# Optimization experiments

Hardware: AMD Instinct MI355X
Metric: run time of the kernel (lower is better)

The kernel has to match this reference:

```python
import jax, jax.numpy as jnp
from jax import lax
import numpy as np

B, N_VARS, M_CLAUSES, K_DIM = 1024, 64, 256, 12
MAX_ITER = 12


def setup_inputs() -> dict:
    key = jax.random.key(0)
    k1, k2, k3, k4 = jax.random.split(key, 4)
    z = jax.random.uniform(k1, (B, N_VARS), dtype=jnp.float32)          # input probabilities
    S = jax.random.normal(k2, (M_CLAUSES, N_VARS + 1), dtype=jnp.float32) * 0.2  # learnable clause matrix (col 0 = truth var)
    w = jax.random.uniform(k3, (M_CLAUSES,), dtype=jnp.float32)          # learnable clause weights
    r = jax.random.normal(k4, (B, N_VARS, K_DIM), dtype=jnp.float32)     # random init directions
    return {"z": z, "S": S, "w": w, "r": r, "max_iter": MAX_ITER}


def _mixing(z, S, w, r, max_iter):
    Bsz, n = z.shape
    m, N = S.shape  # N = n + 1 (truth variable is column 0)
    k = r.shape[-1]
    eps = jnp.float32(1e-8)

    # truth direction v_T = e_0
    vT = jnp.zeros((k,), dtype=z.dtype).at[0].set(1.0)

    # random unit directions orthogonal to v_T (zero out component along e_0)
    r_perp = r.at[..., 0].set(0.0)
    r_perp = r_perp / jnp.maximum(jnp.linalg.norm(r_perp, axis=-1, keepdims=True), eps)

    # SATNet init: v_i = -cos(pi z_i) v_T + sin(pi z_i) r_perp_i
    ang = jnp.pi * z
    Vvars = -jnp.cos(ang)[..., None] * vT + jnp.sin(ang)[..., None] * r_perp  # [B,n,k]
    V = jnp.concatenate([jnp.broadcast_to(vT, (Bsz, 1, k)), Vvars], axis=1)   # [B,N,k]

    Sw = S * w[:, None]                       # weighted clause matrix [m,N]
    W = jnp.einsum('mn,bnk->bmk', Sw, V)      # running product Sw @ V, [B,m,k]
    snrm = jnp.sum(Sw * Sw, axis=0)           # ||s_i||^2 per variable, [N]

    def coord_step(carry, i):
        V, W = carry
        s_i = Sw[:, i]                         # [m]
        v_old = V[:, i, :]                     # [B,k]
        g = jnp.einsum('bmk,m->bk', W, s_i) - snrm[i] * v_old
        v_new = -g / jnp.maximum(jnp.linalg.norm(g, axis=-1, keepdims=True), eps)
        W = W + (v_new - v_old)[:, None, :] * s_i[None, :, None]  # rank-1 update
        V = V.at[:, i, :].set(v_new)
        return (V, W), None

    def sweep(carry, _):
        carry, _ = lax.scan(coord_step, carry, jnp.arange(1, N))  # coordinate descent over variables
        return carry, None

    (V, _), _ = lax.scan(sweep, (V, W), None, length=max_iter)

    # output probabilities: z_i = arccos(-v_i . v_T) / pi
    cos = jnp.clip(-V[:, 1:, 0], -1.0 + 1e-6, 1.0 - 1e-6)
    return jnp.arccos(cos) / jnp.pi


def reference(z, S, w, r, max_iter):
    return _mixing(z, S, w, r, max_iter)
```

## Files before the change

### kernel.cpp

```cpp
#include <hip/hip_runtime.h>
#include <math.h>

#define BATCH 1024
#define NV    64
#define MC    256
#define KD    12
#define PI_F  3.14159265358979323846f

#define C0OFF  4096
#define DGAOFF 4160
#define DGBOFF 4224
#define CBUF   4288

typedef float f2  __attribute__((ext_vector_type(2)));
typedef float v4f __attribute__((ext_vector_type(4)));
typedef __attribute__((address_space(3))) float lds_f;

template <int CTRL>
__device__ __forceinline__ float dpp_addf(float x) {
  int y = __builtin_amdgcn_update_dpp(0, __float_as_int(x), CTRL, 0xF, 0xF, true);
  return x + __int_as_float(y);
}
template <int CTRL>
__device__ __forceinline__ float dpp_movf(float x) {
  return __int_as_float(
      __builtin_amdgcn_update_dpp(0, __float_as_int(x), CTRL, 0xF, 0xF, true));
}
__device__ __forceinline__ float readlane63(float x) {
  return __int_as_float(__builtin_amdgcn_readlane(__float_as_int(x), 63));
}
__device__ __forceinline__ float rlane(float x, int i) {
  return __int_as_float(__builtin_amdgcn_readlane(__float_as_int(x), i));
}

template <int IMM>
__device__ __forceinline__ void dsr(v4f& d, unsigned base) {
  asm volatile("ds_read_b128 %0, %1 offset:%2" : "=v"(d) : "v"(base), "i"(IMM));
}

__global__ void compute_C_kernel(const float* __restrict__ S,
                                 const float* __restrict__ w,
                                 float* __restrict__ Cg, int nsplit) {
  const int q = blockIdx.x;
  const int mc = blockIdx.y;
  const int j = threadIdx.x;
  if (j > NV) return;
  const int v = (q + 1) % 64 + 1;
  const int mlen = MC / nsplit;
  const int m0 = mc * mlen;
  float a0 = 0.f, a1 = 0.f, a2 = 0.f, a3 = 0.f;
  for (int m = m0; m < m0 + mlen; m += 4) {
    const float w0 = w[m], w1 = w[m + 1], w2 = w[m + 2], w3 = w[m + 3];
    a0 = fmaf(S[(m + 0) * (NV + 1) + v] * w0 * w0, S[(m + 0) * (NV + 1) + j], a0);
    a1 = fmaf(S[(m + 1) * (NV + 1) + v] * w1 * w1, S[(m + 1) * (NV + 1) + j], a1);
    a2 = fmaf(S[(m + 2) * (NV + 1) + v] * w2 * w2, S[(m + 2) * (NV + 1) + j], a2);
    a3 = fmaf(S[(m + 3) * (NV + 1) + v] * w3 * w3, S[(m + 3) * (NV + 1) + j], a3);
  }
  const float acc = (a0 + a1) + (a2 + a3);
  float* buf = Cg + mc * CBUF;
  const int p1 = (v == 1) ? 64 : (v - 1);
  const int p2 = (v == 1) ? 63 : (v == 2) ? 64 : (v - 2);
  if (j == 0) buf[C0OFF + q] = acc;
  if (j == p1) buf[DGAOFF + (v - 1)] = acc;
  if (j == p2) buf[DGBOFF + (v - 1)] = acc;
  if (j > 0) {
    const int j0 = j - 1;
    const float st = (j == v || j == p1 || j == p2) ? 0.f : acc;
    buf[q * 64 + (j0 & 3) * 16 + (j0 >> 2)] = st;
  }
}

__global__ __launch_bounds__(256, 1) void mixing_kernel(
    const float* __restrict__ z, const float* __restrict__ r,
    const float* __restrict__ Cg, const int* __restrict__ max_iter_p,
    float* __restrict__ out, int nsplit) {
  __shared__ __align__(16) float Ls[CBUF];

  const int t = threadIdx.x;
  const int l = t & 63;
  const int jg = l & 3;
  const int kk = l >> 2;
  const int b = blockIdx.x * 4 + (t >> 6);
  const int max_iter = max_iter_p[0];

  {
    const float4* src = (const float4*)Cg;
    float4* dst = (float4*)Ls;
    for (int idx = t; idx < CBUF / 4; idx += 256) {
      float4 a = src[idx];
      for (int u = 1; u < nsplit; ++u) {
        const float4 p = src[u * (CBUF / 4) + idx];
        a.x += p.x; a.y += p.y; a.z += p.z; a.w += p.w;
      }
      dst[idx] = a;
    }
  }

  const float my_e0 = (kk == 0) ? 1.f : 0.f;

  f2 Vv[8];
  #pragma unroll
  for (int p = 0; p < 8; ++p) {
    #pragma unroll
    for (int h = 0; h < 2; ++h) {
      const int j0 = jg + 8 * p + 4 * h;
      const float zv = z[b * NV + j0];
      float rp = 0.f;
      if (kk >= 1 && kk < KD) rp = r[(b * NV + j0) * KD + kk];
      float ssp = rp * rp;
      ssp += __shfl_xor(ssp, 4, 64);
      ssp += __shfl_xor(ssp, 8, 64);
      ssp += __shfl_xor(ssp, 16, 64);
      ssp += __shfl_xor(ssp, 32, 64);
      const float inv = 1.f / fmaxf(sqrtf(ssp), 1e-8f);
      const float sn = __builtin_amdgcn_sinf(0.5f * zv);
      const float cs = __builtin_amdgcn_cosf(0.5f * zv);
      const float vv = (kk == 0) ? -cs : sn * rp * inv;
      if (h) Vv[p].y = vv; else Vv[p].x = vv;
    }
  }

  __syncthreads();

  const float t0v = Ls[C0OFF + l];
  const float t1v = Ls[DGAOFF + l];
  const float t2v = Ls[DGBOFF + l];

  float P, vp1, vp2;

  {
    const int rb = 63 * 64 + jg * 16;
    const v4f c0r = *(const v4f*)&Ls[rb + 0];
    const v4f c1r = *(const v4f*)&Ls[rb + 4];
    const v4f c2r = *(const v4f*)&Ls[rb + 8];
    const v4f c3r = *(const v4f*)&Ls[rb + 12];
    f2 qa = (f2){c0r.x, c0r.y} * Vv[0];
    qa = __builtin_elementwise_fma((f2){c0r.z, c0r.w}, Vv[1], qa);
    qa = __builtin_elementwise_fma((f2){c2r.x, c2r.y}, Vv[4], qa);
    qa = __builtin_elementwise_fma((f2){c2r.z, c2r.w}, Vv[5], qa);
    f2 qb = (f2){c1r.x, c1r.y} * Vv[2];
    qb = __builtin_elementwise_fma((f2){c1r.z, c1r.w}, Vv[3], qb);
    qb = __builtin_elementwise_fma((f2){c3r.x, c3r.y}, Vv[6], qb);
    qb = __builtin_elementwise_fma((f2){c3r.z, c3r.w}, Vv[7], qb);
    const f2 qs = qa + qb;
    float q = qs.x + qs.y;
    q = dpp_addf<0xB1>(q);
    q = dpp_addf<0x4E>(q);
    q = fmaf(my_e0, Ls[C0OFF + 63], q);
    P = q;
    vp1 = dpp_movf<0xFF>(Vv[7].y);
    vp2 = dpp_movf<0xAA>(Vv[7].y);
  }

  const unsigned lbase = (unsigned)(unsigned long long)(lds_f*)&Ls[jg * 16];

  v4f Rb[16];

#define PFROW(R) \
  dsr<((((R) & 63) * 256) + 0)>(Rb[(((R) & 3) * 4) + 0], lbase); \
  dsr<((((R) & 63) * 256) + 16)>(Rb[(((R) & 3) * 4) + 1], lbase); \
  dsr<((((R) & 63) * 256) + 32)>(Rb[(((R) & 3) * 4) + 2], lbase); \
  dsr<((((R) & 63) * 256) + 48)>(Rb[(((R) & 3) * 4) + 3], lbase);

#define STEPF(I) { \
  constexpr int i_ = (I); \
  constexpr int j0w_ = (i_ + 63) & 63; \
  constexpr int p_ = j0w_ >> 3; \
  constexpr int h_ = (j0w_ >> 2) & 1; \
  constexpr int jgo_ = j0w_ & 3; \
  constexpr int s_ = (i_ & 3) * 4; \
   \
  asm volatile("s_waitcnt lgkmcnt(8)" ::: "memory"); \
  __builtin_amdgcn_sched_barrier(0); \
  PFROW(i_ + 3) \
  const float da_ = rlane(t1v, i_); \
  const float db_ = rlane(t2v, i_); \
  const float c0_ = rlane(t0v, i_); \
  const float g_ = fmaf(da_, vp1, fmaf(db_, vp2, P)); \
  float t_ = g_ * g_; \
  f2 qa_ = (f2){Rb[s_ + 0].x, Rb[s_ + 0].y} * Vv[0]; \
  qa_ = __builtin_elementwise_fma((f2){Rb[s_ + 0].z, Rb[s_ + 0].w}, Vv[1], qa_); \
  t_ = dpp_addf<0x124>(t_); \
  qa_ = __builtin_elementwise_fma((f2){Rb[s_ + 2].x, Rb[s_ + 2].y}, Vv[4], qa_); \
  qa_ = __builtin_elementwise_fma((f2){Rb[s_ + 2].z, Rb[s_ + 2].w}, Vv[5], qa_); \
  t_ = dpp_addf<0x128>(t_); \
  f2 qb_ = (f2){Rb[s_ + 1].x, Rb[s_ + 1].y} * Vv[2]; \
  qb_ = __builtin_elementwise_fma((f2){Rb[s_ + 1].z, Rb[s_ + 1].w}, Vv[3], qb_); \
  t_ = dpp_addf<0x142>(t_); \
  qb_ = __builtin_elementwise_fma((f2){Rb[s_ + 3].x, Rb[s_ + 3].y}, Vv[6], qb_); \
  qb_ = __builtin_elementwise_fma((f2){Rb[s_ + 3].z, Rb[s_ + 3].w}, Vv[7], qb_); \
  t_ = dpp_addf<0x143>(t_); \
  const f2 qs_ = qa_ + qb_; \
  float q_ = qs_.x + qs_.y; \
  const float n2_ = readlane63(t_); \
  const float inv_ = __builtin_amdgcn_rsqf(fmaxf(n2_, 1e-16f)); \
  q_ = dpp_addf<0xB1>(q_); \
  q_ = dpp_addf<0x4E>(q_); \
  const float vn_ = -g_ * inv_; \
  q_ = fmaf(my_e0, c0_, q_); \
  if constexpr (h_) { Vv[p_].y = (jg == jgo_) ? vp1 : Vv[p_].y; } \
  else              { Vv[p_].x = (jg == jgo_) ? vp1 : Vv[p_].x; } \
  vp2 = vp1; vp1 = vn_; P = q_; \
}

#define S4(N) STEPF((N) + 0) STEPF((N) + 1) STEPF((N) + 2) STEPF((N) + 3)
#define S16(N) S4((N) + 0) S4((N) + 4) S4((N) + 8) S4((N) + 12)

  asm volatile("s_waitcnt lgkmcnt(0)" ::: "memory");
  __builtin_amdgcn_sched_barrier(0);
  PFROW(0) PFROW(1) PFROW(2)

  #pragma unroll 1
  for (int it = 0; it < max_iter; ++it) {
    S16(0) S16(16) S16(32) S16(48)
  }

  Vv[7].y = (jg == 3) ? vp1 : Vv[7].y;

  __syncthreads();
  {
    float* Lw = Ls + (t >> 6) * 64;
    if (kk == 0) {
      Lw[jg +  0] = Vv[0].x; Lw[jg +  4] = Vv[0].y;
      Lw[jg +  8] = Vv[1].x; Lw[jg + 12] = Vv[1].y;
      Lw[jg + 16] = Vv[2].x; Lw[jg + 20] = Vv[2].y;
      Lw[jg + 24] = Vv[3].x; Lw[jg + 28] = Vv[3].y;
      Lw[jg + 32] = Vv[4].x; Lw[jg + 36] = Vv[4].y;
      Lw[jg + 40] = Vv[5].x; Lw[jg + 44] = Vv[5].y;
      Lw[jg + 48] = Vv[6].x; Lw[jg + 52] = Vv[6].y;
      Lw[jg + 56] = Vv[7].x; Lw[jg + 60] = Vv[7].y;
    }
    float cv = -Lw[l];
    cv = fminf(fmaxf(cv, -1.f + 1e-6f), 1.f - 1e-6f);
    out[b * NV + l] = acosf(cv) * (1.f / PI_F);
  }
}

extern "C" void kernel_launch(void* const* d_in, const int* in_sizes, int n_in,
                              void* d_out, int out_size, void* d_ws, size_t ws_size,
                              hipStream_t stream) {
  const float* z = (const float*)d_in[0];
  const float* S = (const float*)d_in[1];
  const float* w = (const float*)d_in[2];
  const float* r = (const float*)d_in[3];
  const int* max_iter = (const int*)d_in[4];
  float* Cg = (float*)d_ws;

  const int nsplit = (ws_size >= (size_t)8 * CBUF * 4) ? 8
                   : (ws_size >= (size_t)4 * CBUF * 4) ? 4 : 1;
  compute_C_kernel<<<dim3(NV, nsplit), 128, 0, stream>>>(S, w, Cg, nsplit);
  mixing_kernel<<<BATCH / 4, 256, 0, stream>>>(z, r, Cg, max_iter,
                                               (float*)d_out, nsplit);
}
```

Measured before the change: 145.5 us.

## Remap wavefront lanes to 16 variables × 4 k-quads per batch element

Changes the thread mapping from 4 variable groups × 16 k-lanes to 16 variable groups × 4 k-quads, so each lane holds 4 k-components for 4 variables. The C-row LDS layout is permuted to match, so each coordinate step needs one ds_read_b128 per lane instead of four, with a 4-slot prefetch ring. The per-step dot product now reduces across 16 lanes with DPP row ops on four accumulators instead of two. This lowers LDS traffic and register use but adds more cross-lane reduction work per step on the serial critical path.

```diff
diff --git a/kernel.cpp b/kernel.cpp
--- a/kernel.cpp
+++ b/kernel.cpp
@@ -20,11 +20,6 @@
 __device__ __forceinline__ float dpp_addf(float x) {
   int y = __builtin_amdgcn_update_dpp(0, __float_as_int(x), CTRL, 0xF, 0xF, true);
   return x + __int_as_float(y);
-}
-template <int CTRL>
-__device__ __forceinline__ float dpp_movf(float x) {
-  return __int_as_float(
-      __builtin_amdgcn_update_dpp(0, __float_as_int(x), CTRL, 0xF, 0xF, true));
 }
 __device__ __forceinline__ float readlane63(float x) {
   return __int_as_float(__builtin_amdgcn_readlane(__float_as_int(x), 63));
@@ -66,7 +61,7 @@
   if (j > 0) {
     const int j0 = j - 1;
     const float st = (j == v || j == p1 || j == p2) ? 0.f : acc;
-    buf[q * 64 + (j0 & 3) * 16 + (j0 >> 2)] = st;
+    buf[q * 64 + (j0 & 15) * 4 + (j0 >> 4)] = st;
   }
 }
 
@@ -78,8 +73,8 @@
 
   const int t = threadIdx.x;
   const int l = t & 63;
-  const int jg = l & 3;
-  const int kk = l >> 2;
+  const int jg = l & 15;
+  const int kq = l >> 4;
   const int b = blockIdx.x * 4 + (t >> 6);
   const int max_iter = max_iter_p[0];
 
@@ -96,28 +91,30 @@
     }
   }
 
-  const float my_e0 = (kk == 0) ? 1.f : 0.f;
-
-  f2 Vv[8];
+  const float my_e0 = (kq == 0) ? 1.f : 0.f;
+
+  f2 Va[4], Vb[4];
   #pragma unroll
-  for (int p = 0; p < 8; ++p) {
-    #pragma unroll
-    for (int h = 0; h < 2; ++h) {
-      const int j0 = jg + 8 * p + 4 * h;
-      const float zv = z[b * NV + j0];
-      float rp = 0.f;
-      if (kk >= 1 && kk < KD) rp = r[(b * NV + j0) * KD + kk];
-      float ssp = rp * rp;
-      ssp += __shfl_xor(ssp, 4, 64);
-      ssp += __shfl_xor(ssp, 8, 64);
-      ssp += __shfl_xor(ssp, 16, 64);
-      ssp += __shfl_xor(ssp, 32, 64);
-      const float inv = 1.f / fmaxf(sqrtf(ssp), 1e-8f);
-      const float sn = __builtin_amdgcn_sinf(0.5f * zv);
-      const float cs = __builtin_amdgcn_cosf(0.5f * zv);
-      const float vv = (kk == 0) ? -cs : sn * rp * inv;
-      if (h) Vv[p].y = vv; else Vv[p].x = vv;
-    }
+  for (int m = 0; m < 4; ++m) {
+    const int j0 = jg + 16 * m;
+    const float zv = z[b * NV + j0];
+    v4f rp4 = {0.f, 0.f, 0.f, 0.f};
+    if (kq < 3) rp4 = *(const v4f*)&r[(b * NV + j0) * KD + 4 * kq];
+    if (kq == 0) rp4.x = 0.f;
+    float ssp = rp4.x * rp4.x;
+    ssp = fmaf(rp4.y, rp4.y, ssp);
+    ssp = fmaf(rp4.z, rp4.z, ssp);
+    ssp = fmaf(rp4.w, rp4.w, ssp);
+    ssp += __shfl_xor(ssp, 16, 64);
+    ssp += __shfl_xor(ssp, 32, 64);
+    const float inv = 1.f / fmaxf(sqrtf(ssp), 1e-8f);
+    const float sn = __builtin_amdgcn_sinf(0.5f * zv);
+    const float cs = __builtin_amdgcn_cosf(0.5f * zv);
+    const float si = sn * inv;
+    Va[m].x = (kq == 0) ? -cs : si * rp4.x;
+    Va[m].y = si * rp4.y;
+    Vb[m].x = si * rp4.z;
+    Vb[m].y = si * rp4.w;
   }
 
   __syncthreads();
@@ -126,88 +123,108 @@
   const float t1v = Ls[DGAOFF + l];
   const float t2v = Ls[DGBOFF + l];
 
-  float P, vp1, vp2;
+  f2 Pa, Pb, vp1a, vp1b, vp2a, vp2b;
 
   {
-    const int rb = 63 * 64 + jg * 16;
-    const v4f c0r = *(const v4f*)&Ls[rb + 0];
-    const v4f c1r = *(const v4f*)&Ls[rb + 4];
-    const v4f c2r = *(const v4f*)&Ls[rb + 8];
-    const v4f c3r = *(const v4f*)&Ls[rb + 12];
-    f2 qa = (f2){c0r.x, c0r.y} * Vv[0];
-    qa = __builtin_elementwise_fma((f2){c0r.z, c0r.w}, Vv[1], qa);
-    qa = __builtin_elementwise_fma((f2){c2r.x, c2r.y}, Vv[4], qa);
-    qa = __builtin_elementwise_fma((f2){c2r.z, c2r.w}, Vv[5], qa);
-    f2 qb = (f2){c1r.x, c1r.y} * Vv[2];
-    qb = __builtin_elementwise_fma((f2){c1r.z, c1r.w}, Vv[3], qb);
-    qb = __builtin_elementwise_fma((f2){c3r.x, c3r.y}, Vv[6], qb);
-    qb = __builtin_elementwise_fma((f2){c3r.z, c3r.w}, Vv[7], qb);
-    const f2 qs = qa + qb;
-    float q = qs.x + qs.y;
-    q = dpp_addf<0xB1>(q);
-    q = dpp_addf<0x4E>(q);
-    q = fmaf(my_e0, Ls[C0OFF + 63], q);
-    P = q;
-    vp1 = dpp_movf<0xFF>(Vv[7].y);
-    vp2 = dpp_movf<0xAA>(Vv[7].y);
-  }
-
-  const unsigned lbase = (unsigned)(unsigned long long)(lds_f*)&Ls[jg * 16];
-
-  v4f Rb[16];
-
-#define PFROW(R) \
-  dsr<((((R) & 63) * 256) + 0)>(Rb[(((R) & 3) * 4) + 0], lbase); \
-  dsr<((((R) & 63) * 256) + 16)>(Rb[(((R) & 3) * 4) + 1], lbase); \
-  dsr<((((R) & 63) * 256) + 32)>(Rb[(((R) & 3) * 4) + 2], lbase); \
-  dsr<((((R) & 63) * 256) + 48)>(Rb[(((R) & 3) * 4) + 3], lbase);
+    const v4f ce = *(const v4f*)&Ls[63 * 64 + jg * 4];
+    f2 qa = (f2){ce.x, ce.x} * Va[0];
+    f2 qb = (f2){ce.x, ce.x} * Vb[0];
+    qa = __builtin_elementwise_fma((f2){ce.y, ce.y}, Va[1], qa);
+    qb = __builtin_elementwise_fma((f2){ce.y, ce.y}, Vb[1], qb);
+    qa = __builtin_elementwise_fma((f2){ce.z, ce.z}, Va[2], qa);
+    qb = __builtin_elementwise_fma((f2){ce.z, ce.z}, Vb[2], qb);
+    qa = __builtin_elementwise_fma((f2){ce.w, ce.w}, Va[3], qa);
+    qb = __builtin_elementwise_fma((f2){ce.w, ce.w}, Vb[3], qb);
+    qa.x = dpp_addf<0xB1>(qa.x); qa.y = dpp_addf<0xB1>(qa.y);
+    qb.x = dpp_addf<0xB1>(qb.x); qb.y = dpp_addf<0xB1>(qb.y);
+    qa.x = dpp_addf<0x4E>(qa.x); qa.y = dpp_addf<0x4E>(qa.y);
+    qb.x = dpp_addf<0x4E>(qb.x); qb.y = dpp_addf<0x4E>(qb.y);
+    qa.x = dpp_addf<0x124>(qa.x); qa.y = dpp_addf<0x124>(qa.y);
+    qb.x = dpp_addf<0x124>(qb.x); qb.y = dpp_addf<0x124>(qb.y);
+    qa.x = dpp_addf<0x128>(qa.x); qa.y = dpp_addf<0x128>(qa.y);
+    qb.x = dpp_addf<0x128>(qb.x); qb.y = dpp_addf<0x128>(qb.y);
+    qa.x = fmaf(my_e0, Ls[C0OFF + 63], qa.x);
+    Pa = qa; Pb = qb;
+    const int rowb = l & 48;
+    vp1a.x = __shfl(Va[3].x, rowb | 15, 64);
+    vp1a.y = __shfl(Va[3].y, rowb | 15, 64);
+    vp1b.x = __shfl(Vb[3].x, rowb | 15, 64);
+    vp1b.y = __shfl(Vb[3].y, rowb | 15, 64);
+    vp2a.x = __shfl(Va[3].x, rowb | 14, 64);
+    vp2a.y = __shfl(Va[3].y, rowb | 14, 64);
+    vp2b.x = __shfl(Vb[3].x, rowb | 14, 64);
+    vp2b.y = __shfl(Vb[3].y, rowb | 14, 64);
+  }
+
+  const unsigned lbase = (unsigned)(unsigned long long)(lds_f*)&Ls[jg * 4];
+
+  v4f Rb[4];
+
+#define PFROW(R) dsr<(((R) & 63) * 256)>(Rb[(R) & 3], lbase);
+
+#define WAITR(SL) asm volatile("s_waitcnt lgkmcnt(2)" : "+v"(Rb[SL]));
 
 #define STEPF(I) { \
   constexpr int i_ = (I); \
   constexpr int j0w_ = (i_ + 63) & 63; \
-  constexpr int p_ = j0w_ >> 3; \
-  constexpr int h_ = (j0w_ >> 2) & 1; \
-  constexpr int jgo_ = j0w_ & 3; \
-  constexpr int s_ = (i_ & 3) * 4; \
-   \
-  asm volatile("s_waitcnt lgkmcnt(8)" ::: "memory"); \
-  __builtin_amdgcn_sched_barrier(0); \
+  constexpr int m_ = j0w_ >> 4; \
+  constexpr int jgo_ = j0w_ & 15; \
+  constexpr int s_ = i_ & 3; \
+  WAITR(s_) \
   PFROW(i_ + 3) \
   const float da_ = rlane(t1v, i_); \
   const float db_ = rlane(t2v, i_); \
   const float c0_ = rlane(t0v, i_); \
-  const float g_ = fmaf(da_, vp1, fmaf(db_, vp2, P)); \
-  float t_ = g_ * g_; \
-  f2 qa_ = (f2){Rb[s_ + 0].x, Rb[s_ + 0].y} * Vv[0]; \
-  qa_ = __builtin_elementwise_fma((f2){Rb[s_ + 0].z, Rb[s_ + 0].w}, Vv[1], qa_); \
-  t_ = dpp_addf<0x124>(t_); \
-  qa_ = __builtin_elementwise_fma((f2){Rb[s_ + 2].x, Rb[s_ + 2].y}, Vv[4], qa_); \
-  qa_ = __builtin_elementwise_fma((f2){Rb[s_ + 2].z, Rb[s_ + 2].w}, Vv[5], qa_); \
-  t_ = dpp_addf<0x128>(t_); \
-  f2 qb_ = (f2){Rb[s_ + 1].x, Rb[s_ + 1].y} * Vv[2]; \
-  qb_ = __builtin_elementwise_fma((f2){Rb[s_ + 1].z, Rb[s_ + 1].w}, Vv[3], qb_); \
+   \
+  f2 ga_ = __builtin_elementwise_fma((f2){db_, db_}, vp2a, Pa); \
+  f2 gb_ = __builtin_elementwise_fma((f2){db_, db_}, vp2b, Pb); \
+  ga_ = __builtin_elementwise_fma((f2){da_, da_}, vp1a, ga_); \
+  gb_ = __builtin_elementwise_fma((f2){da_, da_}, vp1b, gb_); \
+  f2 tp_ = ga_ * ga_; \
+  tp_ = __builtin_elementwise_fma(gb_, gb_, tp_); \
+  float t_ = tp_.x + tp_.y;   \
+   \
+  const v4f ce_ = Rb[s_]; \
+  f2 qa_ = (f2){ce_.x, ce_.x} * Va[0]; \
+  f2 qb_ = (f2){ce_.x, ce_.x} * Vb[0]; \
   t_ = dpp_addf<0x142>(t_); \
-  qb_ = __builtin_elementwise_fma((f2){Rb[s_ + 3].x, Rb[s_ + 3].y}, Vv[6], qb_); \
-  qb_ = __builtin_elementwise_fma((f2){Rb[s_ + 3].z, Rb[s_ + 3].w}, Vv[7], qb_); \
+  qa_ = __builtin_elementwise_fma((f2){ce_.y, ce_.y}, Va[1], qa_); \
+  qb_ = __builtin_elementwise_fma((f2){ce_.y, ce_.y}, Vb[1], qb_); \
   t_ = dpp_addf<0x143>(t_); \
-  const f2 qs_ = qa_ + qb_; \
-  float q_ = qs_.x + qs_.y; \
+  qa_ = __builtin_elementwise_fma((f2){ce_.z, ce_.z}, Va[2], qa_); \
+  qb_ = __builtin_elementwise_fma((f2){ce_.z, ce_.z}, Vb[2], qb_); \
   const float n2_ = readlane63(t_); \
+  qa_ = __builtin_elementwise_fma((f2){ce_.w, ce_.w}, Va[3], qa_); \
+  qb_ = __builtin_elementwise_fma((f2){ce_.w, ce_.w}, Vb[3], qb_); \
   const float inv_ = __builtin_amdgcn_rsqf(fmaxf(n2_, 1e-16f)); \
-  q_ = dpp_addf<0xB1>(q_); \
-  q_ = dpp_addf<0x4E>(q_); \
-  const float vn_ = -g_ * inv_; \
-  q_ = fmaf(my_e0, c0_, q_); \
-  if constexpr (h_) { Vv[p_].y = (jg == jgo_) ? vp1 : Vv[p_].y; } \
-  else              { Vv[p_].x = (jg == jgo_) ? vp1 : Vv[p_].x; } \
-  vp2 = vp1; vp1 = vn_; P = q_; \
+  const f2 ni_ = {-inv_, -inv_}; \
+  const f2 vna_ = ga_ * ni_; \
+  const f2 vnb_ = gb_ * ni_; \
+   \
+  qa_.x = dpp_addf<0xB1>(qa_.x); qa_.y = dpp_addf<0xB1>(qa_.y); \
+  qb_.x = dpp_addf<0xB1>(qb_.x); qb_.y = dpp_addf<0xB1>(qb_.y); \
+  qa_.x = dpp_addf<0x4E>(qa_.x); qa_.y = dpp_addf<0x4E>(qa_.y); \
+  qb_.x = dpp_addf<0x4E>(qb_.x); qb_.y = dpp_addf<0x4E>(qb_.y); \
+  qa_.x = dpp_addf<0x124>(qa_.x); qa_.y = dpp_addf<0x124>(qa_.y); \
+  qb_.x = dpp_addf<0x124>(qb_.x); qb_.y = dpp_addf<0x124>(qb_.y); \
+  qa_.x = dpp_addf<0x128>(qa_.x); qa_.y = dpp_addf<0x128>(qa_.y); \
+  qb_.x = dpp_addf<0x128>(qb_.x); qb_.y = dpp_addf<0x128>(qb_.y); \
+  qa_.x = fmaf(my_e0, c0_, qa_.x); \
+   \
+  Va[m_].x = (jg == jgo_) ? vp1a.x : Va[m_].x; \
+  Va[m_].y = (jg == jgo_) ? vp1a.y : Va[m_].y; \
+  Vb[m_].x = (jg == jgo_) ? vp1b.x : Vb[m_].x; \
+  Vb[m_].y = (jg == jgo_) ? vp1b.y : Vb[m_].y; \
+   \
+  vp2a = vp1a; vp2b = vp1b; \
+  vp1a = vna_; vp1b = vnb_; \
+  Pa = qa_; Pb = qb_; \
 }
 
 #define S4(N) STEPF((N) + 0) STEPF((N) + 1) STEPF((N) + 2) STEPF((N) + 3)
 #define S16(N) S4((N) + 0) S4((N) + 4) S4((N) + 8) S4((N) + 12)
 
   asm volatile("s_waitcnt lgkmcnt(0)" ::: "memory");
-  __builtin_amdgcn_sched_barrier(0);
   PFROW(0) PFROW(1) PFROW(2)
 
   #pragma unroll 1
@@ -215,21 +232,22 @@
     S16(0) S16(16) S16(32) S16(48)
   }
 
-  Vv[7].y = (jg == 3) ? vp1 : Vv[7].y;
-
+  Va[3].x = (jg == 15) ? vp1a.x : Va[3].x;
+  Va[3].y = (jg == 15) ? vp1a.y : Va[3].y;
+  Vb[3].x = (jg == 15) ? vp1b.x : Vb[3].x;
+  Vb[3].y = (jg == 15) ? vp1b.y : Vb[3].y;
+
+  asm volatile("s_waitcnt lgkmcnt(0)" ::: "memory");
   __syncthreads();
   {
     float* Lw = Ls + (t >> 6) * 64;
-    if (kk == 0) {
-      Lw[jg +  0] = Vv[0].x; Lw[jg +  4] = Vv[0].y;
-      Lw[jg +  8] = Vv[1].x; Lw[jg + 12] = Vv[1].y;
-      Lw[jg + 16] = Vv[2].x; Lw[jg + 20] = Vv[2].y;
-      Lw[jg + 24] = Vv[3].x; Lw[jg + 28] = Vv[3].y;
-      Lw[jg + 32] = Vv[4].x; Lw[jg + 36] = Vv[4].y;
-      Lw[jg + 40] = Vv[5].x; Lw[jg + 44] = Vv[5].y;
-      Lw[jg + 48] = Vv[6].x; Lw[jg + 52] = Vv[6].y;
-      Lw[jg + 56] = Vv[7].x; Lw[jg + 60] = Vv[7].y;
+    if (kq == 0) {
+      Lw[jg +  0] = Va[0].x;
+      Lw[jg + 16] = Va[1].x;
+      Lw[jg + 32] = Va[2].x;
+      Lw[jg + 48] = Va[3].x;
     }
+    __builtin_amdgcn_s_waitcnt(0);
     float cv = -Lw[l];
     cv = fminf(fmaxf(cv, -1.f + 1e-6f), 1.f - 1e-6f);
     out[b * NV + l] = acosf(cv) * (1.f / PI_F);
```

After: 160.4 us. 10.2% more time.
